# Performance work log

Hardware: AMD Instinct MI355X
Metric: run time of the kernel (lower is better)

The kernel has to match this reference:

```python
import jax, jax.numpy as jnp
import numpy as np

D_MODEL = 1024
NUM_HEADS = 16
HEAD_DIM = D_MODEL // NUM_HEADS
BATCH = 4
SEQ = 2048


def circulant(x, c, b):
    # Circulant linear layer via FFT: y = irfft(rfft(x) * rfft(c)) + b
    # x: (..., d), c: (d,), b: (d,)
    d = c.shape[0]
    y = jnp.fft.irfft(jnp.fft.rfft(x, axis=-1) * jnp.fft.rfft(c), n=d, axis=-1)
    return y + b


def setup_inputs() -> dict:
    key = jax.random.key(0)
    ks = jax.random.split(key, 9)
    scale = 1.0 / np.sqrt(D_MODEL)
    inp = {
        "x": jax.random.normal(ks[0], (BATCH, SEQ, D_MODEL), dtype=jnp.float32),
        "wq_c": jax.random.normal(ks[1], (D_MODEL,), dtype=jnp.float32) * scale,
        "wq_b": jnp.zeros((D_MODEL,), dtype=jnp.float32),
        "wk_c": jax.random.normal(ks[2], (D_MODEL,), dtype=jnp.float32) * scale,
        "wk_b": jnp.zeros((D_MODEL,), dtype=jnp.float32),
        "wv_c": jax.random.normal(ks[3], (D_MODEL,), dtype=jnp.float32) * scale,
        "wv_b": jnp.zeros((D_MODEL,), dtype=jnp.float32),
        "wo_c": jax.random.normal(ks[4], (D_MODEL,), dtype=jnp.float32) * scale,
        "wo_b": jnp.zeros((D_MODEL,), dtype=jnp.float32),
    }
    return inp


def reference(x, wq_c, wq_b, wk_c, wk_b, wv_c, wv_b, wo_c, wo_b):
    bs, seq_len, dm = x.shape
    Q = circulant(x, wq_c, wq_b)  # (B, S, D)
    K = circulant(x, wk_c, wk_b)
    V = circulant(x, wv_c, wv_b)
    Q = Q.reshape(bs, seq_len, NUM_HEADS, HEAD_DIM)
    K = K.reshape(bs, seq_len, NUM_HEADS, HEAD_DIM)
    V = V.reshape(bs, seq_len, NUM_HEADS, HEAD_DIM)
    scale = HEAD_DIM ** (-0.5)
    attn_logits = jnp.einsum("bqhd,bkhd->bhqk", Q, K) * scale  # (B, H, S, S)
    attn_weights = jax.nn.softmax(attn_logits, axis=-1)
    out_heads = jnp.einsum("bhqk,bkhd->bqhd", attn_weights, V)
    out_merge = out_heads.reshape(bs, seq_len, dm)
    out = circulant(out_merge, wo_c, wo_b)
    return out
```

## Files before the change

### kernel.cpp

```cpp
#include <hip/hip_runtime.h>
#include <hip/hip_bf16.h>

#define D_MODEL 1024
#define NUM_HEADS 16
#define HEAD_DIM 64
#define BATCH 4
#define SEQ 2048
#define MROWS (BATCH * SEQ)

using f32x4  = __attribute__((ext_vector_type(4))) float;
using bf16x8 = __attribute__((ext_vector_type(8))) short;
using short4v = __attribute__((ext_vector_type(4))) short;

__device__ inline unsigned short f2bf(float f) {
    __hip_bfloat16 h = __float2bfloat16(f);
    return *reinterpret_cast<unsigned short*>(&h);
}

__device__ inline void gld_lds16(const unsigned short* g, unsigned short* l) {
    __builtin_amdgcn_global_load_lds(
        (const __attribute__((address_space(1))) unsigned int*)g,
        (__attribute__((address_space(3))) unsigned int*)l, 16, 0, 0);
}

#define QSCALE 0.18033688011112042f

__global__ __launch_bounds__(256) void build_w(
    const float* __restrict__ cq, const float* __restrict__ ck,
    const float* __restrict__ cv, const float* __restrict__ co,
    const float* __restrict__ bq, const float* __restrict__ bk,
    const float* __restrict__ bv, const float* __restrict__ bo,
    unsigned short* __restrict__ Wt, float* __restrict__ bias)
{
    const int n = blockIdx.x;
    const int sel = n >> 10, nl = n & 1023;
    const float* c  = sel == 0 ? cq : sel == 1 ? ck : sel == 2 ? cv : co;
    const float* bb = sel == 0 ? bq : sel == 1 ? bk : sel == 2 ? bv : bo;
    const float sc = (sel == 0) ? QSCALE : 1.0f;
    const int t = threadIdx.x;
    ushort4 o;
    o.x = f2bf(sc * c[(nl - (4*t + 0)) & 1023]);
    o.y = f2bf(sc * c[(nl - (4*t + 1)) & 1023]);
    o.z = f2bf(sc * c[(nl - (4*t + 2)) & 1023]);
    o.w = f2bf(sc * c[(nl - (4*t + 3)) & 1023]);
    ((ushort4*)(Wt + (size_t)n * 1024))[t] = o;
    if (t == 0) bias[n] = sc * bb[nl];
}

__global__ __launch_bounds__(256) void xcast(
    const float* __restrict__ x, unsigned short* __restrict__ xb)
{
    const size_t i = (size_t)blockIdx.x * 1024 + threadIdx.x * 4;
    float4 v = *(const float4*)(x + i);
    ushort4 o;
    o.x = f2bf(v.x); o.y = f2bf(v.y); o.z = f2bf(v.z); o.w = f2bf(v.w);
    *(ushort4*)(xb + i) = o;
}

template <int OUT_MODE>
__global__ __launch_bounds__(256, 3) void gemm_circ(
    const unsigned short* __restrict__ A,
    const unsigned short* __restrict__ Bt,
    const float* __restrict__ bias,
    unsigned short* __restrict__ Qb, unsigned short* __restrict__ Kb,
    unsigned short* __restrict__ Vt, float* __restrict__ Cf)
{
    __shared__ unsigned short As[128 * 64];
    __shared__ unsigned short Bs[128 * 64];
    const int t = threadIdx.x;
    const int w = t >> 6, lane = t & 63;
    const int quad = lane >> 4, l16 = lane & 15;
    const int m0 = blockIdx.x * 128;
    const int n0 = blockIdx.y * 128;
    const int wm = (w & 1) * 64, wn = (w >> 1) * 64;

    f32x4 acc[4][4];
#pragma unroll
    for (int i = 0; i < 4; ++i)
#pragma unroll
        for (int j = 0; j < 4; ++j) acc[i][j] = (f32x4){0.f, 0.f, 0.f, 0.f};

    for (int k0 = 0; k0 < 1024; k0 += 64) {
        __syncthreads();
#pragma unroll
        for (int j = 0; j < 4; ++j) {
            const int s = j * 4 + w;
            const int i = s * 64 + lane;
            const int r = i >> 3;
            const int c = (i & 7) ^ (r & 7);
            gld_lds16(A  + (size_t)(m0 + r) * 1024 + k0 + c * 8, &As[s * 512]);
            gld_lds16(Bt + (size_t)(n0 + r) * 1024 + k0 + c * 8, &Bs[s * 512]);
        }
        __syncthreads();

#pragma unroll
        for (int kk = 0; kk < 2; ++kk) {
            bf16x8 af[4], bfr[4];
#pragma unroll
            for (int i = 0; i < 4; ++i) {
                const int r = wm + i * 16 + l16;
                const int slot = r * 8 + ((kk * 4 + quad) ^ (r & 7));
                af[i] = *(const bf16x8*)&As[slot * 8];
            }
#pragma unroll
            for (int j = 0; j < 4; ++j) {
                const int r = wn + j * 16 + l16;
                const int slot = r * 8 + ((kk * 4 + quad) ^ (r & 7));
                bfr[j] = *(const bf16x8*)&Bs[slot * 8];
            }
#pragma unroll
            for (int i = 0; i < 4; ++i)
#pragma unroll
                for (int j = 0; j < 4; ++j)
                    acc[i][j] = __builtin_amdgcn_mfma_f32_16x16x32_bf16(
                        af[i], bfr[j], acc[i][j], 0, 0, 0);
        }
    }

#pragma unroll
    for (int i = 0; i < 4; ++i) {
        const int gm = m0 + wm + i * 16 + quad * 4;
#pragma unroll
        for (int j = 0; j < 4; ++j) {
            const int gn = n0 + wn + j * 16 + l16;
            const float bv = bias[gn];
            if (OUT_MODE == 1) {
#pragma unroll
                for (int rr = 0; rr < 4; ++rr)
                    Cf[(size_t)(gm + rr) * 1024 + gn] = acc[i][j][rr] + bv;
            } else {
                const int sel = gn >> 10;
                if (sel == 0) {
#pragma unroll
                    for (int rr = 0; rr < 4; ++rr)
                        Qb[(size_t)(gm + rr) * 1024 + gn] = f2bf(acc[i][j][rr] + bv);
                } else if (sel == 1) {
                    const int col = gn & 1023;
#pragma unroll
                    for (int rr = 0; rr < 4; ++rr)
                        Kb[(size_t)(gm + rr) * 1024 + col] = f2bf(acc[i][j][rr] + bv);
                } else {
                    const int d = gn & 1023;
                    const int head = d >> 6, dl = d & 63;
                    const int b = gm >> 11, key = gm & 2047;
                    ushort4 vv;
                    vv.x = f2bf(acc[i][j][0] + bv);
                    vv.y = f2bf(acc[i][j][1] + bv);
                    vv.z = f2bf(acc[i][j][2] + bv);
                    vv.w = f2bf(acc[i][j][3] + bv);
                    *(ushort4*)&Vt[((size_t)((b * 16 + head) * 64 + dl)) * 2048 + key] = vv;
                }
            }
        }
    }
}

__global__ __launch_bounds__(256, 2) void attn_mfma(
    const unsigned short* __restrict__ Qb, const unsigned short* __restrict__ Kb,
    const unsigned short* __restrict__ Vt, unsigned short* __restrict__ O)
{
    __shared__ unsigned short Ks[2][64 * 64];
    __shared__ unsigned short Vs[2][64 * 64];

    const int t = threadIdx.x;
    const int w = t >> 6, lane = t & 63;
    const int quad = lane >> 4, l16 = lane & 15;
    const int bh = blockIdx.x;
    const int b = bh >> 4, head = bh & 15;
    const int qbase = blockIdx.y * 256 + w * 64;

    bf16x8 qa[4][2];
#pragma unroll
    for (int s = 0; s < 4; ++s)
#pragma unroll
        for (int h = 0; h < 2; ++h) {
            size_t off = (size_t)(b * SEQ + qbase + s*16 + l16) * D_MODEL
                       + head * HEAD_DIM + h*32 + quad*8;
            qa[s][h] = *(const bf16x8*)(Qb + off);
        }

    f32x4 acc[4][4];
#pragma unroll
    for (int s = 0; s < 4; ++s)
#pragma unroll
        for (int dt = 0; dt < 4; ++dt) acc[s][dt] = (f32x4){0.f,0.f,0.f,0.f};
    float lp[4] = {0.f, 0.f, 0.f, 0.f};

    const size_t kbase  = (size_t)(b * SEQ) * D_MODEL + head * HEAD_DIM;
    const size_t vtbase = (size_t)((b * NUM_HEADS + head) * HEAD_DIM) * SEQ;

#pragma unroll
    for (int j = 0; j < 2; ++j) {
        const int seg = j * 4 + w;
        const int i = seg * 64 + lane;
        const int r = i >> 3;
        const int ck = (i & 7) ^ ((r & 3) | ((r >> 1) & 4));
        const int cv = (i & 7) ^ (r & 7);
        gld_lds16(Kb + kbase + (size_t)r * D_MODEL + ck * 8, &Ks[0][seg * 512]);
        gld_lds16(Vt + vtbase + (size_t)r * SEQ + cv * 8, &Vs[0][seg * 512]);
    }

    int ib = 0;
    for (int kb = 0; kb < SEQ; kb += 64, ib ^= 1) {
        __syncthreads();

        if (kb + 64 < SEQ) {
#pragma unroll
            for (int j = 0; j < 2; ++j) {
                const int seg = j * 4 + w;
                const int i = seg * 64 + lane;
                const int r = i >> 3;
                const int ck = (i & 7) ^ ((r & 3) | ((r >> 1) & 4));
                const int cv = (i & 7) ^ (r & 7);
                gld_lds16(Kb + kbase + (size_t)(kb + 64 + r) * D_MODEL + ck * 8,
                          &Ks[ib ^ 1][seg * 512]);
                gld_lds16(Vt + vtbase + (size_t)r * SEQ + kb + 64 + cv * 8,
                          &Vs[ib ^ 1][seg * 512]);
            }
        }

        bf16x8 kf[2][2][2];
#pragma unroll
        for (int kh = 0; kh < 2; ++kh)
#pragma unroll
            for (int m = 0; m < 2; ++m) {
                const int r = kh * 32 + ((l16 >> 2) << 3) + m * 4 + (l16 & 3);
                const int sg = (r & 3) | ((r >> 1) & 4);
#pragma unroll
                for (int h = 0; h < 2; ++h) {
                    const int cc = (h * 4 + quad) ^ sg;
                    kf[kh][m][h] = *(const bf16x8*)&Ks[ib][(r * 8 + cc) * 8];
                }
            }

#pragma unroll
        for (int kh = 0; kh < 2; ++kh) {
            bf16x8 pf[4];
#pragma unroll
            for (int s = 0; s < 4; ++s) {
                f32x4 st0 = (f32x4){0.f,0.f,0.f,0.f};
                f32x4 st1 = (f32x4){0.f,0.f,0.f,0.f};
#pragma unroll
                for (int h = 0; h < 2; ++h) {
                    st0 = __builtin_amdgcn_mfma_f32_16x16x32_bf16(
                        kf[kh][0][h], qa[s][h], st0, 0, 0, 0);
                    st1 = __builtin_amdgcn_mfma_f32_16x16x32_bf16(
                        kf[kh][1][h], qa[s][h], st1, 0, 0, 0);
                }
                float p0 = __builtin_amdgcn_exp2f(st0[0]);
                float p1 = __builtin_amdgcn_exp2f(st0[1]);
                float p2 = __builtin_amdgcn_exp2f(st0[2]);
                float p3 = __builtin_amdgcn_exp2f(st0[3]);
                float p4 = __builtin_amdgcn_exp2f(st1[0]);
                float p5 = __builtin_amdgcn_exp2f(st1[1]);
                float p6 = __builtin_amdgcn_exp2f(st1[2]);
                float p7 = __builtin_amdgcn_exp2f(st1[3]);
                lp[s] += ((p0 + p1) + (p2 + p3)) + ((p4 + p5) + (p6 + p7));
                __hip_bfloat162 w0 = __float22bfloat162_rn(make_float2(p0, p1));
                __hip_bfloat162 w1 = __float22bfloat162_rn(make_float2(p2, p3));
                __hip_bfloat162 w2 = __float22bfloat162_rn(make_float2(p4, p5));
                __hip_bfloat162 w3 = __float22bfloat162_rn(make_float2(p6, p7));
                union { bf16x8 v; unsigned int u[4]; } pu;
                pu.u[0] = *reinterpret_cast<unsigned int*>(&w0);
                pu.u[1] = *reinterpret_cast<unsigned int*>(&w1);
                pu.u[2] = *reinterpret_cast<unsigned int*>(&w2);
                pu.u[3] = *reinterpret_cast<unsigned int*>(&w3);
                pf[s] = pu.v;
            }

#pragma unroll
            for (int dt = 0; dt < 4; ++dt) {
                const int r = dt * 16 + l16;
                const int cv = (kh * 4 + quad) ^ (r & 7);
                bf16x8 vf = *(const bf16x8*)&Vs[ib][(r * 8 + cv) * 8];
#pragma unroll
                for (int s = 0; s < 4; ++s)
                    acc[s][dt] = __builtin_amdgcn_mfma_f32_16x16x32_bf16(
                        pf[s], vf, acc[s][dt], 0, 0, 0);
            }
        }
    }

#pragma unroll
    for (int s = 0; s < 4; ++s) {
        lp[s] += __shfl_xor(lp[s], 16);
        lp[s] += __shfl_xor(lp[s], 32);
    }

#pragma unroll
    for (int s = 0; s < 4; ++s)
#pragma unroll
        for (int rr = 0; rr < 4; ++rr) {
            float denom = __shfl(lp[s], quad * 4 + rr);
            float inv = 1.0f / denom;
            int q = qbase + s*16 + quad*4 + rr;
            unsigned short* orow = O + (size_t)(b * SEQ + q) * D_MODEL + head * HEAD_DIM + l16;
#pragma unroll
            for (int dt = 0; dt < 4; ++dt) orow[dt*16] = f2bf(acc[s][dt][rr] * inv);
        }
}

extern "C" void kernel_launch(void* const* d_in, const int* in_sizes, int n_in,
                              void* d_out, int out_size, void* d_ws, size_t ws_size,
                              hipStream_t stream) {
    const float* x    = (const float*)d_in[0];
    const float* wq_c = (const float*)d_in[1];
    const float* wq_b = (const float*)d_in[2];
    const float* wk_c = (const float*)d_in[3];
    const float* wk_b = (const float*)d_in[4];
    const float* wv_c = (const float*)d_in[5];
    const float* wv_b = (const float*)d_in[6];
    const float* wo_c = (const float*)d_in[7];
    const float* wo_b = (const float*)d_in[8];
    float* out = (float*)d_out;

    char* ws = (char*)d_ws;
    unsigned short* Wt   = (unsigned short*)(ws);
    float*          bias = (float*)(ws + ((size_t)8  << 20));
    unsigned short* xb   = (unsigned short*)(ws + ((size_t)10 << 20));
    unsigned short* Qb   = (unsigned short*)(ws + ((size_t)26 << 20));
    unsigned short* Kb   = (unsigned short*)(ws + ((size_t)42 << 20));
    unsigned short* Vt   = (unsigned short*)(ws + ((size_t)58 << 20));
    unsigned short* Ob   = (unsigned short*)(ws + ((size_t)74 << 20));

    build_w<<<4096, 256, 0, stream>>>(wq_c, wk_c, wv_c, wo_c,
                                      wq_b, wk_b, wv_b, wo_b, Wt, bias);
    xcast<<<MROWS, 256, 0, stream>>>(x, xb);
    gemm_circ<0><<<dim3(64, 24), 256, 0, stream>>>(xb, Wt, bias, Qb, Kb, Vt, nullptr);
    attn_mfma<<<dim3(BATCH * NUM_HEADS, SEQ / 256), 256, 0, stream>>>(Qb, Kb, Vt, Ob);
    gemm_circ<1><<<dim3(64, 8), 256, 0, stream>>>(Ob, Wt + (size_t)3072 * 1024,
                                                  bias + 3072, nullptr, nullptr, nullptr, out);
}
```

Baseline: 247.0 us.

## Load K and V fragments directly from global memory instead of LDS

The attention kernel no longer stages K and V tiles in shared memory through async global-to-LDS copies and barriers. Each wave now loads its K fragments straight into registers, double-buffered in registers through a two-step unrolled loop, and loads its V fragments from global memory just before use. This removes the LDS traffic and the per-tile __syncthreads. In exchange, the four waves of a block each fetch the same K/V data separately, which raises global and L2 traffic, and V loads are no longer prefetched ahead of use. Register pressure also rises.

```diff
diff --git a/kernel.cpp b/kernel.cpp
--- a/kernel.cpp
+++ b/kernel.cpp
@@ -10,7 +10,6 @@
 
 using f32x4  = __attribute__((ext_vector_type(4))) float;
 using bf16x8 = __attribute__((ext_vector_type(8))) short;
-using short4v = __attribute__((ext_vector_type(4))) short;
 
 __device__ inline unsigned short f2bf(float f) {
     __hip_bfloat16 h = __float2bfloat16(f);
@@ -159,9 +158,6 @@
     const unsigned short* __restrict__ Qb, const unsigned short* __restrict__ Kb,
     const unsigned short* __restrict__ Vt, unsigned short* __restrict__ O)
 {
-    __shared__ unsigned short Ks[2][64 * 64];
-    __shared__ unsigned short Vs[2][64 * 64];
-
     const int t = threadIdx.x;
     const int w = t >> 6, lane = t & 63;
     const int quad = lane >> 4, l16 = lane & 15;
@@ -186,55 +182,44 @@
         for (int dt = 0; dt < 4; ++dt) acc[s][dt] = (f32x4){0.f,0.f,0.f,0.f};
     float lp[4] = {0.f, 0.f, 0.f, 0.f};
 
-    const size_t kbase  = (size_t)(b * SEQ) * D_MODEL + head * HEAD_DIM;
-    const size_t vtbase = (size_t)((b * NUM_HEADS + head) * HEAD_DIM) * SEQ;
-
-#pragma unroll
-    for (int j = 0; j < 2; ++j) {
-        const int seg = j * 4 + w;
-        const int i = seg * 64 + lane;
-        const int r = i >> 3;
-        const int ck = (i & 7) ^ ((r & 3) | ((r >> 1) & 4));
-        const int cv = (i & 7) ^ (r & 7);
-        gld_lds16(Kb + kbase + (size_t)r * D_MODEL + ck * 8, &Ks[0][seg * 512]);
-        gld_lds16(Vt + vtbase + (size_t)r * SEQ + cv * 8, &Vs[0][seg * 512]);
-    }
-
-    int ib = 0;
-    for (int kb = 0; kb < SEQ; kb += 64, ib ^= 1) {
-        __syncthreads();
-
+    const unsigned short* Kh = Kb + (size_t)(b * SEQ) * D_MODEL + head * HEAD_DIM;
+    const unsigned short* Vh = Vt + (size_t)((b * NUM_HEADS + head) * HEAD_DIM) * SEQ;
+
+    const int krow = ((l16 >> 2) << 3) + (l16 & 3);
+    const int dq = quad * 8;
+
+    bf16x8 kfA[2][2][2], kfB[2][2][2];
+
+#pragma unroll
+    for (int kh = 0; kh < 2; ++kh)
+#pragma unroll
+        for (int m = 0; m < 2; ++m)
+#pragma unroll
+            for (int h = 0; h < 2; ++h)
+                kfA[kh][m][h] = *(const bf16x8*)(
+                    Kh + (size_t)(kh*32 + krow + m*4) * D_MODEL + h*32 + dq);
+
+    auto body = [&](int kb, bf16x8 (&kfc)[2][2][2], bf16x8 (&kfn)[2][2][2]) {
         if (kb + 64 < SEQ) {
 #pragma unroll
-            for (int j = 0; j < 2; ++j) {
-                const int seg = j * 4 + w;
-                const int i = seg * 64 + lane;
-                const int r = i >> 3;
-                const int ck = (i & 7) ^ ((r & 3) | ((r >> 1) & 4));
-                const int cv = (i & 7) ^ (r & 7);
-                gld_lds16(Kb + kbase + (size_t)(kb + 64 + r) * D_MODEL + ck * 8,
-                          &Ks[ib ^ 1][seg * 512]);
-                gld_lds16(Vt + vtbase + (size_t)r * SEQ + kb + 64 + cv * 8,
-                          &Vs[ib ^ 1][seg * 512]);
-            }
-        }
-
-        bf16x8 kf[2][2][2];
-#pragma unroll
-        for (int kh = 0; kh < 2; ++kh)
-#pragma unroll
-            for (int m = 0; m < 2; ++m) {
-                const int r = kh * 32 + ((l16 >> 2) << 3) + m * 4 + (l16 & 3);
-                const int sg = (r & 3) | ((r >> 1) & 4);
-#pragma unroll
-                for (int h = 0; h < 2; ++h) {
-                    const int cc = (h * 4 + quad) ^ sg;
-                    kf[kh][m][h] = *(const bf16x8*)&Ks[ib][(r * 8 + cc) * 8];
-                }
-            }
+            for (int kh = 0; kh < 2; ++kh)
+#pragma unroll
+                for (int m = 0; m < 2; ++m)
+#pragma unroll
+                    for (int h = 0; h < 2; ++h)
+                        kfn[kh][m][h] = *(const bf16x8*)(
+                            Kh + (size_t)(kb + 64 + kh*32 + krow + m*4) * D_MODEL
+                               + h*32 + dq);
+        }
 
 #pragma unroll
         for (int kh = 0; kh < 2; ++kh) {
+            bf16x8 vfr[4];
+#pragma unroll
+            for (int dt = 0; dt < 4; ++dt)
+                vfr[dt] = *(const bf16x8*)(
+                    Vh + (size_t)(dt*16 + l16) * SEQ + kb + kh*32 + dq);
+
             bf16x8 pf[4];
 #pragma unroll
             for (int s = 0; s < 4; ++s) {
@@ -243,9 +228,9 @@
 #pragma unroll
                 for (int h = 0; h < 2; ++h) {
                     st0 = __builtin_amdgcn_mfma_f32_16x16x32_bf16(
-                        kf[kh][0][h], qa[s][h], st0, 0, 0, 0);
+                        kfc[kh][0][h], qa[s][h], st0, 0, 0, 0);
                     st1 = __builtin_amdgcn_mfma_f32_16x16x32_bf16(
-                        kf[kh][1][h], qa[s][h], st1, 0, 0, 0);
+                        kfc[kh][1][h], qa[s][h], st1, 0, 0, 0);
                 }
                 float p0 = __builtin_amdgcn_exp2f(st0[0]);
                 float p1 = __builtin_amdgcn_exp2f(st0[1]);
@@ -269,16 +254,17 @@
             }
 
 #pragma unroll
-            for (int dt = 0; dt < 4; ++dt) {
-                const int r = dt * 16 + l16;
-                const int cv = (kh * 4 + quad) ^ (r & 7);
-                bf16x8 vf = *(const bf16x8*)&Vs[ib][(r * 8 + cv) * 8];
+            for (int dt = 0; dt < 4; ++dt)
 #pragma unroll
                 for (int s = 0; s < 4; ++s)
                     acc[s][dt] = __builtin_amdgcn_mfma_f32_16x16x32_bf16(
-                        pf[s], vf, acc[s][dt], 0, 0, 0);
-            }
-        }
+                        pf[s], vfr[dt], acc[s][dt], 0, 0, 0);
+        }
+    };
+
+    for (int kb = 0; kb < SEQ; kb += 128) {
+        body(kb,      kfA, kfB);
+        body(kb + 64, kfB, kfA);
     }
 
 #pragma unroll
```

Result: slower. 316.1 us (+28.0%).
